# Kernel tuning notes

Hardware: AMD Instinct MI355X
Metric: run time of the kernel (lower is better)

## Reference

```python
import jax, jax.numpy as jnp
import numpy as np

B, T, E, H, V, O = 64, 512, 128, 256, 100000, 1


def setup_inputs() -> dict:
    key = jax.random.key(0)
    ks = jax.random.split(key, 10)
    sE, sH = 1.0 / np.sqrt(E), 1.0 / np.sqrt(H)
    return {
        "x": jax.random.randint(ks[0], (B, T), 0, V),
        "emb_table": jax.random.normal(ks[1], (V, E), jnp.float32) * 0.1,
        "W_ih": jax.random.normal(ks[2], (4 * H, E), jnp.float32) * sE,  # torch gate order i,f,g,o
        "W_hh": jax.random.normal(ks[3], (4 * H, H), jnp.float32) * sH,
        "b_ih": jnp.zeros((4 * H,), jnp.float32),  # biases init'd to 0 in source
        "b_hh": jnp.zeros((4 * H,), jnp.float32),
        "Wm": jax.random.normal(ks[4], (H, H), jnp.float32) * sH,
        "bm": jnp.zeros((H,), jnp.float32),
        "Wf": jax.random.normal(ks[5], (O, H), jnp.float32) * sH,
        "bf": jnp.zeros((O,), jnp.float32),
    }


def reference(x, emb_table, W_ih, W_hh, b_ih, b_hh, Wm, bm, Wf, bf):
    batch = x.shape[0]
    hid = W_hh.shape[1]
    # vectorized replacement for the per-(i,j) python-loop embedding copy
    embeds = emb_table[x]                                  # [B,T,E]
    # precompute input contribution to all gates for every timestep
    gx = jnp.einsum('bte,ge->btg', embeds, W_ih) + b_ih     # [B,T,4H]
    gx = jnp.swapaxes(gx, 0, 1)                             # [T,B,4H]
    h0 = jnp.zeros((batch, hid), embeds.dtype)
    c0 = jnp.zeros((batch, hid), embeds.dtype)

    def step(carry, g_t):
        h, c = carry
        g = g_t + h @ W_hh.T + b_hh                         # [B,4H]
        i, f, gg, o = jnp.split(g, 4, axis=-1)
        i, f, o = jax.nn.sigmoid(i), jax.nn.sigmoid(f), jax.nn.sigmoid(o)
        c = f * c + i * jnp.tanh(gg)
        h = o * jnp.tanh(c)
        return (h, c), h

    (hT, cT), hs = jax.lax.scan(step, (h0, c0), gx)
    out = jnp.swapaxes(hs, 0, 1)                            # [B,T,H]
    out = out @ Wm.T + bm                                   # ffmiddle
    out = out @ Wf.T + bf                                   # fc -> [B,T,O]
    sig_out = jax.nn.sigmoid(out).reshape(batch, -1).mean(axis=1)  # [B]
    # hidden = (h_n, c_n) with leading num_layers=1 dim, as in torch
    return sig_out, hT[None, :, :], cT[None, :, :]
```

## Files before the change

kernel.cpp:

```cpp
#include <hip/hip_runtime.h>


#define BATCH 64
#define TSTEPS 512
#define EDIM 128
#define HDIM 256
#define G4H 1024

typedef short bf16x8 __attribute__((ext_vector_type(8)));
typedef short bf16x4 __attribute__((ext_vector_type(4)));
typedef float f32x4 __attribute__((ext_vector_type(4)));

__device__ __forceinline__ unsigned short f2bf(float f) {
  unsigned u = __builtin_bit_cast(unsigned, f);
  return (unsigned short)((u + 0x7fffu + ((u >> 16) & 1u)) >> 16);
}
__device__ __forceinline__ float bf2f(unsigned short h) {
  unsigned u = ((unsigned)h) << 16;
  return __builtin_bit_cast(float, u);
}
__device__ __forceinline__ unsigned pk2(float a, float b) {
  return (unsigned)f2bf(a) | ((unsigned)f2bf(b) << 16);
}
__device__ __forceinline__ float fsig(float x) {
  return __builtin_amdgcn_rcpf(1.f + __expf(-x));
}
__device__ __forceinline__ float ftanh(float x) {
  return 1.f - 2.f * __builtin_amdgcn_rcpf(__expf(2.f * x) + 1.f);
}
__device__ __forceinline__ bf16x8 ldfrag(const unsigned short* p) {
  bf16x4 a = *(const bf16x4*)p;
  bf16x4 b = *(const bf16x4*)(p + 16);
  return __builtin_shufflevector(a, b, 0, 1, 2, 3, 4, 5, 6, 7);
}
__device__ __forceinline__ bf16x8 pack8(float4 v0, float4 v1) {
  bf16x8 f;
  f[0] = (short)f2bf(v0.x); f[1] = (short)f2bf(v0.y);
  f[2] = (short)f2bf(v0.z); f[3] = (short)f2bf(v0.w);
  f[4] = (short)f2bf(v1.x); f[5] = (short)f2bf(v1.y);
  f[6] = (short)f2bf(v1.z); f[7] = (short)f2bf(v1.w);
  return f;
}

__global__ __launch_bounds__(256) void k_gx(const int* __restrict__ x,
                                            const float* __restrict__ emb,
                                            const float* __restrict__ Wih,
                                            const float* __restrict__ bih,
                                            unsigned short* __restrict__ gx3) {
  const int t = blockIdx.x;
  const int g0 = blockIdx.y * 64;
  const int tid = threadIdx.x;
  __shared__ unsigned short Al[64 * 136];
  __shared__ unsigned short Bl[64 * 136];
  __shared__ int tok[64];
  if (tid < 64) tok[tid] = x[tid * TSTEPS + t];
  __syncthreads();
  {
    const int r = tid >> 2, c0 = (tid & 3) * 32;
    const float* asrc = emb + (size_t)tok[r] * EDIM + c0;
    const float* bsrc = Wih + (size_t)(g0 + r) * EDIM + c0;
#pragma unroll
    for (int s = 0; s < 32; s += 8) {
      float4 a0 = *(const float4*)(asrc + s);
      float4 a1 = *(const float4*)(asrc + s + 4);
      uint4 pa = {pk2(a0.x, a0.y), pk2(a0.z, a0.w), pk2(a1.x, a1.y), pk2(a1.z, a1.w)};
      *(uint4*)&Al[r * 136 + c0 + s] = pa;
      float4 b0 = *(const float4*)(bsrc + s);
      float4 b1 = *(const float4*)(bsrc + s + 4);
      uint4 pb = {pk2(b0.x, b0.y), pk2(b0.z, b0.w), pk2(b1.x, b1.y), pk2(b1.z, b1.w)};
      *(uint4*)&Bl[r * 136 + c0 + s] = pb;
    }
  }
  __syncthreads();
  const int lane = tid & 63, w = tid >> 6;
  const int lo = lane & 15, hi = lane >> 4;
  const int mb = (w & 1) * 32, nb = (w >> 1) * 32;
  f32x4 acc[2][2];
#pragma unroll
  for (int jj = 0; jj < 2; ++jj) {
    float bv = bih[g0 + nb + jj * 16 + lo];
    acc[0][jj] = (f32x4){bv, bv, bv, bv};
    acc[1][jj] = acc[0][jj];
  }
#pragma unroll
  for (int kk = 0; kk < 4; ++kk) {
    bf16x8 af0 = ldfrag(&Al[(mb + lo) * 136 + kk * 32 + hi * 4]);
    bf16x8 af1 = ldfrag(&Al[(mb + 16 + lo) * 136 + kk * 32 + hi * 4]);
    bf16x8 bf0 = ldfrag(&Bl[(nb + lo) * 136 + kk * 32 + hi * 4]);
    bf16x8 bf1 = ldfrag(&Bl[(nb + 16 + lo) * 136 + kk * 32 + hi * 4]);
    acc[0][0] = __builtin_amdgcn_mfma_f32_16x16x32_bf16(af0, bf0, acc[0][0], 0, 0, 0);
    acc[0][1] = __builtin_amdgcn_mfma_f32_16x16x32_bf16(af0, bf1, acc[0][1], 0, 0, 0);
    acc[1][0] = __builtin_amdgcn_mfma_f32_16x16x32_bf16(af1, bf0, acc[1][0], 0, 0, 0);
    acc[1][1] = __builtin_amdgcn_mfma_f32_16x16x32_bf16(af1, bf1, acc[1][1], 0, 0, 0);
  }
#pragma unroll
  for (int i = 0; i < 2; ++i)
#pragma unroll
    for (int jj = 0; jj < 2; ++jj) {
      int grp = (w & 1) * 2 + i;
      int col = g0 + nb + jj * 16 + lo;
      int g = col >> 8, jc = col & 255;
      int halfb = jc >> 7, wv = (jc >> 4) & 7, lov = jc & 15;
      size_t base = (((size_t)(t * 8 + grp * 2 + halfb) * 8 + wv) * 64 +
                     (hi * 16 + lov)) * 16 + g * 4;
      unsigned long long val =
          (unsigned long long)pk2(acc[i][jj][0], acc[i][jj][1]) |
          ((unsigned long long)pk2(acc[i][jj][2], acc[i][jj][3]) << 32);
      *(unsigned long long*)&gx3[base] = val;
    }
}

__global__ __launch_bounds__(512, 2) void k_rec(const unsigned short* __restrict__ gx3,
                                                const float* __restrict__ Whh,
                                                const float* __restrict__ bhh,
                                                const float* __restrict__ weff,
                                                unsigned long long* __restrict__ hx,
                                                float* __restrict__ out) {
  const int tid = threadIdx.x;
  const int bp = blockIdx.x;
  const int grp = bp >> 1, half = bp & 1;
  const int b0 = grp * 16;
  const int lane = tid & 63, w = tid >> 6;
  const int lo = lane & 15, hi = lane >> 4;
  const int j = half * 128 + w * 16 + lo;
  __shared__ unsigned short h_lds[2][32 * 136];
  bf16x8 wf[4][8];
  float bhv[4];
#pragma unroll
  for (int g = 0; g < 4; ++g) {
    const float* wr = Whh + (size_t)(g * 256 + j) * HDIM;
    bhv[g] = bhh[g * 256 + j];
#pragma unroll
    for (int kk = 0; kk < 8; ++kk) {
      const float* p = wr + kk * 32 + hi * 8;
      wf[g][kk] = pack8(*(const float4*)p, *(const float4*)(p + 4));
    }
  }
  const int hb_b = tid >> 5, hb_g = tid & 31;
  float wv8[8];
#pragma unroll
  for (int e = 0; e < 8; ++e) wv8[e] = weff[hb_g * 8 + e];
  const float c0 = weff[256];
  float sig_acc = 0.f;
  for (int i = tid; i < 32 * 136 / 2; i += 512) ((unsigned*)h_lds[0])[i] = 0u;
  const unsigned short* gp = gx3 + (((size_t)bp * 8 + w) * 64 + lane) * 16;
  unsigned gwA[8], gwB[8];
  {
    uint4 a = *(const uint4*)(gp);
    uint4 b = *(const uint4*)(gp + 8);
    gwA[0] = a.x; gwA[1] = a.y; gwA[2] = a.z; gwA[3] = a.w;
    gwA[4] = b.x; gwA[5] = b.y; gwA[6] = b.z; gwA[7] = b.w;
    uint4 c2 = *(const uint4*)(gp + 65536);
    uint4 d2 = *(const uint4*)(gp + 65536 + 8);
    gwB[0] = c2.x; gwB[1] = c2.y; gwB[2] = c2.z; gwB[3] = c2.w;
    gwB[4] = d2.x; gwB[5] = d2.y; gwB[6] = d2.z; gwB[7] = d2.w;
  }
  float c[4] = {0.f, 0.f, 0.f, 0.f};
  float hv[4];
  const int ob = (j >> 3) * 136 + (j & 7);
  const int jp = ((half ^ 1) * 128) + ((tid >> 6) << 4) + (tid & 15);
  const int hip = (tid >> 4) & 3;
  const int pb = (jp >> 3) * 136 + (jp & 7);
  __syncthreads();
  auto step = [&](int t, unsigned (&G)[8]) {
    const int cur = t & 1, nxt = cur ^ 1;
    const unsigned wt = (unsigned)(t + 1);
    f32x4 acc[4];
#pragma unroll
    for (int g = 0; g < 4; ++g)
#pragma unroll
      for (int r = 0; r < 4; ++r) {
        unsigned word = G[g * 2 + (r >> 1)];
        unsigned short v = (r & 1) ? (unsigned short)(word >> 16) : (unsigned short)word;
        acc[g][r] = bf2f(v) + bhv[g];
      }
#pragma unroll
    for (int kk = 0; kk < 8; ++kk) {
      bf16x8 a = *(const bf16x8*)&h_lds[cur][(kk * 4 + hi) * 136 + lo * 8];
      acc[0] = __builtin_amdgcn_mfma_f32_16x16x32_bf16(a, wf[0][kk], acc[0], 0, 0, 0);
      acc[1] = __builtin_amdgcn_mfma_f32_16x16x32_bf16(a, wf[1][kk], acc[1], 0, 0, 0);
      acc[2] = __builtin_amdgcn_mfma_f32_16x16x32_bf16(a, wf[2][kk], acc[2], 0, 0, 0);
      acc[3] = __builtin_amdgcn_mfma_f32_16x16x32_bf16(a, wf[3][kk], acc[3], 0, 0, 0);
    }
    unsigned short hbf[4];
#pragma unroll
    for (int r = 0; r < 4; ++r) {
      float iv = fsig(acc[0][r]), fv = fsig(acc[1][r]);
      float gv = ftanh(acc[2][r]), ov = fsig(acc[3][r]);
      c[r] = fv * c[r] + iv * gv;
      hv[r] = ov * ftanh(c[r]);
      hbf[r] = f2bf(hv[r]);
    }
    const int par = (int)(wt & 1u);
    {
      const unsigned long long tg = ((unsigned long long)wt) << 32;
      unsigned long long* dst = &hx[((size_t)(par * 8 + bp)) * 1024 + w * 128 + lane * 2];
      __hip_atomic_store(&dst[0], tg | (unsigned long long)pk2(hv[0], hv[1]),
                         __ATOMIC_RELAXED, __HIP_MEMORY_SCOPE_AGENT);
      __hip_atomic_store(&dst[1], tg | (unsigned long long)pk2(hv[2], hv[3]),
                         __ATOMIC_RELAXED, __HIP_MEMORY_SCOPE_AGENT);
      asm volatile("" ::: "memory");
    }
#pragma unroll
    for (int r = 0; r < 4; ++r) h_lds[nxt][ob + (hi * 4 + r) * 8] = hbf[r];
    unsigned long long v0, v1;
    {
      unsigned long long* src = &hx[((size_t)(par * 8 + (bp ^ 1))) * 1024 + tid * 2];
      do {
        v0 = __hip_atomic_load(&src[0], __ATOMIC_RELAXED, __HIP_MEMORY_SCOPE_AGENT);
        v1 = __hip_atomic_load(&src[1], __ATOMIC_RELAXED, __HIP_MEMORY_SCOPE_AGENT);
      } while ((unsigned)(v0 >> 32) != wt || (unsigned)(v1 >> 32) != wt);
    }
    if (t + 2 < TSTEPS) {
      const unsigned short* q = gp + (size_t)(t + 2) * 65536;
      uint4 a = *(const uint4*)(q);
      uint4 b = *(const uint4*)(q + 8);
      G[0] = a.x; G[1] = a.y; G[2] = a.z; G[3] = a.w;
      G[4] = b.x; G[5] = b.y; G[6] = b.z; G[7] = b.w;
    }
    h_lds[nxt][pb + (hip * 4 + 0) * 8] = (unsigned short)v0;
    h_lds[nxt][pb + (hip * 4 + 1) * 8] = (unsigned short)(v0 >> 16);
    h_lds[nxt][pb + (hip * 4 + 2) * 8] = (unsigned short)v1;
    h_lds[nxt][pb + (hip * 4 + 3) * 8] = (unsigned short)(v1 >> 16);
    __syncthreads();
    {
      bf16x8 hh = *(const bf16x8*)&h_lds[nxt][hb_g * 136 + hb_b * 8];
      float s = 0.f;
#pragma unroll
      for (int e = 0; e < 8; ++e) s += bf2f((unsigned short)hh[e]) * wv8[e];
      s += __shfl_xor(s, 1);  s += __shfl_xor(s, 2);  s += __shfl_xor(s, 4);
      s += __shfl_xor(s, 8);  s += __shfl_xor(s, 16);
      sig_acc += fsig(s + c0);
    }
  };
  for (int t = 0; t < TSTEPS; t += 2) {
    step(t, gwA);
    step(t + 1, gwB);
  }
  if (half == 0 && hb_g == 0) out[b0 + hb_b] = sig_acc * (1.f / 512.f);
#pragma unroll
  for (int r = 0; r < 4; ++r) {
    const int b = b0 + hi * 4 + r;
    out[64 + b * HDIM + j] = hv[r];
    out[64 + BATCH * HDIM + b * HDIM + j] = c[r];
  }
}

__global__ __launch_bounds__(256) void k_weff(const float* __restrict__ Wm,
                                              const float* __restrict__ bm,
                                              const float* __restrict__ Wf,
                                              const float* __restrict__ bfb,
                                              float* __restrict__ weff) {
  const int k = threadIdx.x;
  __shared__ float red[256];
  float acc = 0.f;
#pragma unroll 8
  for (int jj = 0; jj < 256; ++jj) acc += Wf[jj] * Wm[jj * 256 + k];
  weff[k] = acc;
  red[k] = bm[k] * Wf[k];
  __syncthreads();
  for (int s = 128; s > 0; s >>= 1) {
    if (k < s) red[k] += red[k + s];
    __syncthreads();
  }
  if (k == 0) weff[256] = red[0] + bfb[0];
}

extern "C" void kernel_launch(void* const* d_in, const int* in_sizes, int n_in,
                              void* d_out, int out_size, void* d_ws, size_t ws_size,
                              hipStream_t stream) {
  (void)in_sizes; (void)n_in; (void)out_size; (void)ws_size;
  const int* x = (const int*)d_in[0];
  const float* emb = (const float*)d_in[1];
  const float* Wih = (const float*)d_in[2];
  const float* Whh = (const float*)d_in[3];
  const float* bih = (const float*)d_in[4];
  const float* bhh = (const float*)d_in[5];
  const float* Wm  = (const float*)d_in[6];
  const float* bm  = (const float*)d_in[7];
  const float* Wf  = (const float*)d_in[8];
  const float* bf  = (const float*)d_in[9];
  float* out = (float*)d_out;
  char* ws = (char*)d_ws;
  const size_t gx_bytes = (size_t)TSTEPS * BATCH * G4H * 2;
  const size_t hx_bytes = (size_t)2 * 8 * 1024 * 8;
  unsigned short* gx3 = (unsigned short*)ws;
  unsigned long long* hx = (unsigned long long*)(ws + gx_bytes);
  float* weff = (float*)(ws + gx_bytes + hx_bytes);
  hipMemsetAsync(hx, 0, hx_bytes, stream);
  k_gx<<<dim3(512, 16), 256, 0, stream>>>(x, emb, Wih, bih, gx3);
  k_weff<<<1, 256, 0, stream>>>(Wm, bm, Wf, bf, weff);
  k_rec<<<8, 512, 0, stream>>>(gx3, Whh, bhh, weff, hx, out);
}
```

Baseline: 1.197 ms.

## Split recurrent MFMA into own/partner halves to overlap with cross-block exchange

Each LSTM step's h@W_hh product is split into the K-half this block computes itself and the half received from the partner block. The own-half MFMAs for the next step now run before polling for the partner's hidden state, and the head reduction is moved into that gap. This hides exchange latency behind compute. The poll loop is also software-pipelined with two outstanding load pairs. It adds a second barrier per step and a more intricate prologue and epilogue, which brings some risk of ordering mistakes.

```diff
diff --git a/kernel.cpp b/kernel.cpp
--- a/kernel.cpp
+++ b/kernel.cpp
@@ -144,28 +144,27 @@
   float sig_acc = 0.f;
   for (int i = tid; i < 32 * 136 / 2; i += 512) ((unsigned*)h_lds[0])[i] = 0u;
   const unsigned short* gp = gx3 + (((size_t)bp * 8 + w) * 64 + lane) * 16;
-  unsigned gwA[8], gwB[8];
+  unsigned gwE[8], gwO[8];
   {
     uint4 a = *(const uint4*)(gp);
     uint4 b = *(const uint4*)(gp + 8);
-    gwA[0] = a.x; gwA[1] = a.y; gwA[2] = a.z; gwA[3] = a.w;
-    gwA[4] = b.x; gwA[5] = b.y; gwA[6] = b.z; gwA[7] = b.w;
+    gwE[0] = a.x; gwE[1] = a.y; gwE[2] = a.z; gwE[3] = a.w;
+    gwE[4] = b.x; gwE[5] = b.y; gwE[6] = b.z; gwE[7] = b.w;
     uint4 c2 = *(const uint4*)(gp + 65536);
     uint4 d2 = *(const uint4*)(gp + 65536 + 8);
-    gwB[0] = c2.x; gwB[1] = c2.y; gwB[2] = c2.z; gwB[3] = c2.w;
-    gwB[4] = d2.x; gwB[5] = d2.y; gwB[6] = d2.z; gwB[7] = d2.w;
+    gwO[0] = c2.x; gwO[1] = c2.y; gwO[2] = c2.z; gwO[3] = c2.w;
+    gwO[4] = d2.x; gwO[5] = d2.y; gwO[6] = d2.z; gwO[7] = d2.w;
   }
   float c[4] = {0.f, 0.f, 0.f, 0.f};
   float hv[4];
+  f32x4 acc[4];
   const int ob = (j >> 3) * 136 + (j & 7);
   const int jp = ((half ^ 1) * 128) + ((tid >> 6) << 4) + (tid & 15);
   const int hip = (tid >> 4) & 3;
   const int pb = (jp >> 3) * 136 + (jp & 7);
   __syncthreads();
-  auto step = [&](int t, unsigned (&G)[8]) {
-    const int cur = t & 1, nxt = cur ^ 1;
-    const unsigned wt = (unsigned)(t + 1);
-    f32x4 acc[4];
+
+  auto cinit = [&](const unsigned (&G)[8]) {
 #pragma unroll
     for (int g = 0; g < 4; ++g)
 #pragma unroll
@@ -174,14 +173,47 @@
         unsigned short v = (r & 1) ? (unsigned short)(word >> 16) : (unsigned short)word;
         acc[g][r] = bf2f(v) + bhv[g];
       }
-#pragma unroll
-    for (int kk = 0; kk < 8; ++kk) {
-      bf16x8 a = *(const bf16x8*)&h_lds[cur][(kk * 4 + hi) * 136 + lo * 8];
-      acc[0] = __builtin_amdgcn_mfma_f32_16x16x32_bf16(a, wf[0][kk], acc[0], 0, 0, 0);
-      acc[1] = __builtin_amdgcn_mfma_f32_16x16x32_bf16(a, wf[1][kk], acc[1], 0, 0, 0);
-      acc[2] = __builtin_amdgcn_mfma_f32_16x16x32_bf16(a, wf[2][kk], acc[2], 0, 0, 0);
-      acc[3] = __builtin_amdgcn_mfma_f32_16x16x32_bf16(a, wf[3][kk], acc[3], 0, 0, 0);
-    }
+  };
+  auto mfma_own = [&](int buf) {
+    if (half == 0) {
+#pragma unroll
+      for (int kk = 0; kk < 4; ++kk) {
+        bf16x8 a = *(const bf16x8*)&h_lds[buf][(kk * 4 + hi) * 136 + lo * 8];
+#pragma unroll
+        for (int g = 0; g < 4; ++g)
+          acc[g] = __builtin_amdgcn_mfma_f32_16x16x32_bf16(a, wf[g][kk], acc[g], 0, 0, 0);
+      }
+    } else {
+#pragma unroll
+      for (int kk = 4; kk < 8; ++kk) {
+        bf16x8 a = *(const bf16x8*)&h_lds[buf][(kk * 4 + hi) * 136 + lo * 8];
+#pragma unroll
+        for (int g = 0; g < 4; ++g)
+          acc[g] = __builtin_amdgcn_mfma_f32_16x16x32_bf16(a, wf[g][kk], acc[g], 0, 0, 0);
+      }
+    }
+  };
+  auto mfma_par = [&](int buf) {
+    if (half == 0) {
+#pragma unroll
+      for (int kk = 4; kk < 8; ++kk) {
+        bf16x8 a = *(const bf16x8*)&h_lds[buf][(kk * 4 + hi) * 136 + lo * 8];
+#pragma unroll
+        for (int g = 0; g < 4; ++g)
+          acc[g] = __builtin_amdgcn_mfma_f32_16x16x32_bf16(a, wf[g][kk], acc[g], 0, 0, 0);
+      }
+    } else {
+#pragma unroll
+      for (int kk = 0; kk < 4; ++kk) {
+        bf16x8 a = *(const bf16x8*)&h_lds[buf][(kk * 4 + hi) * 136 + lo * 8];
+#pragma unroll
+        for (int g = 0; g < 4; ++g)
+          acc[g] = __builtin_amdgcn_mfma_f32_16x16x32_bf16(a, wf[g][kk], acc[g], 0, 0, 0);
+      }
+    }
+  };
+  auto update_store = [&](int t) {
+    const unsigned wt = (unsigned)(t + 1);
     unsigned short hbf[4];
 #pragma unroll
     for (int r = 0; r < 4; ++r) {
@@ -192,51 +224,80 @@
       hbf[r] = f2bf(hv[r]);
     }
     const int par = (int)(wt & 1u);
-    {
-      const unsigned long long tg = ((unsigned long long)wt) << 32;
-      unsigned long long* dst = &hx[((size_t)(par * 8 + bp)) * 1024 + w * 128 + lane * 2];
-      __hip_atomic_store(&dst[0], tg | (unsigned long long)pk2(hv[0], hv[1]),
-                         __ATOMIC_RELAXED, __HIP_MEMORY_SCOPE_AGENT);
-      __hip_atomic_store(&dst[1], tg | (unsigned long long)pk2(hv[2], hv[3]),
-                         __ATOMIC_RELAXED, __HIP_MEMORY_SCOPE_AGENT);
-      asm volatile("" ::: "memory");
-    }
-#pragma unroll
-    for (int r = 0; r < 4; ++r) h_lds[nxt][ob + (hi * 4 + r) * 8] = hbf[r];
+    unsigned long long* dst = &hx[((size_t)(par * 8 + bp)) * 1024 + w * 128 + lane * 2];
+    const unsigned long long tg = ((unsigned long long)wt) << 32;
+    __hip_atomic_store(&dst[0], tg | (unsigned long long)pk2(hv[0], hv[1]),
+                       __ATOMIC_RELAXED, __HIP_MEMORY_SCOPE_AGENT);
+    __hip_atomic_store(&dst[1], tg | (unsigned long long)pk2(hv[2], hv[3]),
+                       __ATOMIC_RELAXED, __HIP_MEMORY_SCOPE_AGENT);
+    asm volatile("" ::: "memory");
+#pragma unroll
+    for (int r = 0; r < 4; ++r) h_lds[par][ob + (hi * 4 + r) * 8] = hbf[r];
+  };
+  auto head = [&](int buf) {
+    bf16x8 hh = *(const bf16x8*)&h_lds[buf][hb_g * 136 + hb_b * 8];
+    float s = 0.f;
+#pragma unroll
+    for (int e = 0; e < 8; ++e) s += bf2f((unsigned short)hh[e]) * wv8[e];
+    s += __shfl_xor(s, 1);  s += __shfl_xor(s, 2);  s += __shfl_xor(s, 4);
+    s += __shfl_xor(s, 8);  s += __shfl_xor(s, 16);
+    sig_acc += fsig(s + c0);
+  };
+  auto gx_issue = [&](int s, unsigned (&G)[8]) {
+    const unsigned short* q = gp + (size_t)s * 65536;
+    uint4 a = *(const uint4*)(q);
+    uint4 b = *(const uint4*)(q + 8);
+    G[0] = a.x; G[1] = a.y; G[2] = a.z; G[3] = a.w;
+    G[4] = b.x; G[5] = b.y; G[6] = b.z; G[7] = b.w;
+  };
+  auto poll_write = [&](int t) {
+    const unsigned wt = (unsigned)(t + 1);
+    const int par = (int)(wt & 1u);
+    unsigned long long* src = &hx[((size_t)(par * 8 + (bp ^ 1))) * 1024 + tid * 2];
+    unsigned long long a0 = __hip_atomic_load(&src[0], __ATOMIC_RELAXED, __HIP_MEMORY_SCOPE_AGENT);
+    unsigned long long a1 = __hip_atomic_load(&src[1], __ATOMIC_RELAXED, __HIP_MEMORY_SCOPE_AGENT);
+    unsigned long long b0 = __hip_atomic_load(&src[0], __ATOMIC_RELAXED, __HIP_MEMORY_SCOPE_AGENT);
+    unsigned long long b1 = __hip_atomic_load(&src[1], __ATOMIC_RELAXED, __HIP_MEMORY_SCOPE_AGENT);
     unsigned long long v0, v1;
-    {
-      unsigned long long* src = &hx[((size_t)(par * 8 + (bp ^ 1))) * 1024 + tid * 2];
-      do {
-        v0 = __hip_atomic_load(&src[0], __ATOMIC_RELAXED, __HIP_MEMORY_SCOPE_AGENT);
-        v1 = __hip_atomic_load(&src[1], __ATOMIC_RELAXED, __HIP_MEMORY_SCOPE_AGENT);
-      } while ((unsigned)(v0 >> 32) != wt || (unsigned)(v1 >> 32) != wt);
-    }
-    if (t + 2 < TSTEPS) {
-      const unsigned short* q = gp + (size_t)(t + 2) * 65536;
-      uint4 a = *(const uint4*)(q);
-      uint4 b = *(const uint4*)(q + 8);
-      G[0] = a.x; G[1] = a.y; G[2] = a.z; G[3] = a.w;
-      G[4] = b.x; G[5] = b.y; G[6] = b.z; G[7] = b.w;
-    }
-    h_lds[nxt][pb + (hip * 4 + 0) * 8] = (unsigned short)v0;
-    h_lds[nxt][pb + (hip * 4 + 1) * 8] = (unsigned short)(v0 >> 16);
-    h_lds[nxt][pb + (hip * 4 + 2) * 8] = (unsigned short)v1;
-    h_lds[nxt][pb + (hip * 4 + 3) * 8] = (unsigned short)(v1 >> 16);
+    for (;;) {
+      if ((unsigned)(a0 >> 32) == wt && (unsigned)(a1 >> 32) == wt) { v0 = a0; v1 = a1; break; }
+      a0 = b0; a1 = b1;
+      b0 = __hip_atomic_load(&src[0], __ATOMIC_RELAXED, __HIP_MEMORY_SCOPE_AGENT);
+      b1 = __hip_atomic_load(&src[1], __ATOMIC_RELAXED, __HIP_MEMORY_SCOPE_AGENT);
+    }
+    h_lds[par][pb + (hip * 4 + 0) * 8] = (unsigned short)v0;
+    h_lds[par][pb + (hip * 4 + 1) * 8] = (unsigned short)(v0 >> 16);
+    h_lds[par][pb + (hip * 4 + 2) * 8] = (unsigned short)v1;
+    h_lds[par][pb + (hip * 4 + 3) * 8] = (unsigned short)(v1 >> 16);
+  };
+  auto body = [&](int t, unsigned (&Gc)[8], unsigned (&Gf)[8]) {
+    mfma_par(t & 1);
+    update_store(t);
+    if (t + 2 < TSTEPS) gx_issue(t + 2, Gf);
     __syncthreads();
-    {
-      bf16x8 hh = *(const bf16x8*)&h_lds[nxt][hb_g * 136 + hb_b * 8];
-      float s = 0.f;
-#pragma unroll
-      for (int e = 0; e < 8; ++e) s += bf2f((unsigned short)hh[e]) * wv8[e];
-      s += __shfl_xor(s, 1);  s += __shfl_xor(s, 2);  s += __shfl_xor(s, 4);
-      s += __shfl_xor(s, 8);  s += __shfl_xor(s, 16);
-      sig_acc += fsig(s + c0);
-    }
-  };
-  for (int t = 0; t < TSTEPS; t += 2) {
-    step(t, gwA);
-    step(t + 1, gwB);
-  }
+    if (t < TSTEPS - 1) {
+      cinit(Gc);
+      mfma_own((t + 1) & 1);
+    }
+    head(t & 1);
+    poll_write(t);
+    __syncthreads();
+  };
+
+  cinit(gwE);
+  update_store(0);
+  gx_issue(2, gwE);
+  __syncthreads();
+  cinit(gwO);
+  mfma_own(1);
+  poll_write(0);
+  __syncthreads();
+  for (int t = 1; t + 1 < TSTEPS - 1; t += 2) {
+    body(t, gwE, gwO);
+    body(t + 1, gwO, gwE);
+  }
+  body(TSTEPS - 1, gwE, gwO);
+  head(0);
   if (half == 0 && hb_g == 0) out[b0 + hb_b] = sig_acc * (1.f / 512.f);
 #pragma unroll
   for (int r = 0; r < 4; ++r) {
```

Result: faster. 1.034 ms, median of 2 (-13.6%).

## Quantize recurrent matmul to int8 MFMA and drop cross-block hidden exchange

Applied to the files above, without the earlier changes.

The recurrence kernel now quantizes W_hh per row to int8 and the hidden state per step to int8 with a dynamic block-wide max scale, using i8 MFMA instead of bf16. Each block owns all 256 hidden units for 16 batch rows, so the two-block split with atomic spin-wait exchange through global memory is removed and only 4 blocks launch. The b_hh bias is folded into the precomputed input gates. This removes the inter-block synchronisation latency per step but adds an extra __syncthreads for the max reduction and introduces int8 quantization error in the recurrence.

```diff
diff --git a/kernel.cpp b/kernel.cpp
--- a/kernel.cpp
+++ b/kernel.cpp
@@ -10,6 +10,7 @@
 typedef short bf16x8 __attribute__((ext_vector_type(8)));
 typedef short bf16x4 __attribute__((ext_vector_type(4)));
 typedef float f32x4 __attribute__((ext_vector_type(4)));
+typedef int i32x4 __attribute__((ext_vector_type(4)));
 
 __device__ __forceinline__ unsigned short f2bf(float f) {
   unsigned u = __builtin_bit_cast(unsigned, f);
@@ -33,20 +34,18 @@
   bf16x4 b = *(const bf16x4*)(p + 16);
   return __builtin_shufflevector(a, b, 0, 1, 2, 3, 4, 5, 6, 7);
 }
-__device__ __forceinline__ bf16x8 pack8(float4 v0, float4 v1) {
-  bf16x8 f;
-  f[0] = (short)f2bf(v0.x); f[1] = (short)f2bf(v0.y);
-  f[2] = (short)f2bf(v0.z); f[3] = (short)f2bf(v0.w);
-  f[4] = (short)f2bf(v1.x); f[5] = (short)f2bf(v1.y);
-  f[6] = (short)f2bf(v1.z); f[7] = (short)f2bf(v1.w);
-  return f;
+__device__ __forceinline__ int q8(float v, float qs) {
+  float r = __builtin_rintf(v * qs);
+  r = fmaxf(-127.f, fminf(127.f, r));
+  return (int)r;
 }
 
 __global__ __launch_bounds__(256) void k_gx(const int* __restrict__ x,
                                             const float* __restrict__ emb,
                                             const float* __restrict__ Wih,
                                             const float* __restrict__ bih,
-                                            unsigned short* __restrict__ gx3) {
+                                            const float* __restrict__ bhh,
+                                            unsigned short* __restrict__ gx4) {
   const int t = blockIdx.x;
   const int g0 = blockIdx.y * 64;
   const int tid = threadIdx.x;
@@ -78,7 +77,8 @@
   f32x4 acc[2][2];
 #pragma unroll
   for (int jj = 0; jj < 2; ++jj) {
-    float bv = bih[g0 + nb + jj * 16 + lo];
+    const int col = g0 + nb + jj * 16 + lo;
+    float bv = bih[col] + bhh[col];
     acc[0][jj] = (f32x4){bv, bv, bv, bv};
     acc[1][jj] = acc[0][jj];
   }
@@ -97,153 +97,182 @@
   for (int i = 0; i < 2; ++i)
 #pragma unroll
     for (int jj = 0; jj < 2; ++jj) {
-      int grp = (w & 1) * 2 + i;
-      int col = g0 + nb + jj * 16 + lo;
-      int g = col >> 8, jc = col & 255;
-      int halfb = jc >> 7, wv = (jc >> 4) & 7, lov = jc & 15;
-      size_t base = (((size_t)(t * 8 + grp * 2 + halfb) * 8 + wv) * 64 +
-                     (hi * 16 + lov)) * 16 + g * 4;
+      const int o = (w & 1) * 2 + i;
+      const int col = g0 + nb + jj * 16 + lo;
+      const int g = col >> 8, rem = col & 255;
+      const int w4 = rem >> 5, t2 = (rem >> 4) & 1;
+      size_t idx = ((((size_t)t * 4 + o) * 8 + w4) * 64 + (hi * 16 + lo)) * 32 +
+                   (g * 2 + t2) * 4;
       unsigned long long val =
           (unsigned long long)pk2(acc[i][jj][0], acc[i][jj][1]) |
           ((unsigned long long)pk2(acc[i][jj][2], acc[i][jj][3]) << 32);
-      *(unsigned long long*)&gx3[base] = val;
-    }
-}
-
-__global__ __launch_bounds__(512, 2) void k_rec(const unsigned short* __restrict__ gx3,
-                                                const float* __restrict__ Whh,
-                                                const float* __restrict__ bhh,
-                                                const float* __restrict__ weff,
-                                                unsigned long long* __restrict__ hx,
-                                                float* __restrict__ out) {
+      *(unsigned long long*)&gx4[idx] = val;
+    }
+}
+
+__global__ __launch_bounds__(512) void k_rec(const unsigned short* __restrict__ gx4,
+                                             const float* __restrict__ Whh,
+                                             const float* __restrict__ weff,
+                                             float* __restrict__ out) {
   const int tid = threadIdx.x;
-  const int bp = blockIdx.x;
-  const int grp = bp >> 1, half = bp & 1;
-  const int b0 = grp * 16;
+  const int blk = blockIdx.x;
   const int lane = tid & 63, w = tid >> 6;
   const int lo = lane & 15, hi = lane >> 4;
-  const int j = half * 128 + w * 16 + lo;
-  __shared__ unsigned short h_lds[2][32 * 136];
-  bf16x8 wf[4][8];
-  float bhv[4];
-#pragma unroll
-  for (int g = 0; g < 4; ++g) {
-    const float* wr = Whh + (size_t)(g * 256 + j) * HDIM;
-    bhv[g] = bhh[g * 256 + j];
-#pragma unroll
-    for (int kk = 0; kk < 8; ++kk) {
-      const float* p = wr + kk * 32 + hi * 8;
-      wf[g][kk] = pack8(*(const float4*)p, *(const float4*)(p + 4));
-    }
-  }
-  const int hb_b = tid >> 5, hb_g = tid & 31;
+  __shared__ unsigned char h8[2][16 * 272];
+  __shared__ float mxl[8];
+  i32x4 wq[4][2][4];
+  float sW[4][2];
+#pragma unroll
+  for (int g = 0; g < 4; ++g)
+#pragma unroll
+    for (int t2 = 0; t2 < 2; ++t2) {
+      const float* wr = Whh + (size_t)(g * 256 + w * 32 + t2 * 16 + lo) * HDIM;
+      float m = 0.f;
+#pragma unroll 16
+      for (int e = 0; e < 64; ++e) {
+        float4 v = *(const float4*)(wr + e * 4);
+        m = fmaxf(m, fmaxf(fmaxf(fabsf(v.x), fabsf(v.y)),
+                           fmaxf(fabsf(v.z), fabsf(v.w))));
+      }
+      m = fmaxf(m, 1e-20f);
+      sW[g][t2] = m * (1.f / 127.f);
+      const float qs = 127.f / m;
+#pragma unroll
+      for (int kk = 0; kk < 4; ++kk) {
+        int wd[4];
+#pragma unroll
+        for (int u2 = 0; u2 < 4; ++u2) {
+          float4 v = *(const float4*)(wr + kk * 64 + hi * 16 + u2 * 4);
+          int b0 = q8(v.x, qs), b1 = q8(v.y, qs), b2 = q8(v.z, qs), b3 = q8(v.w, qs);
+          wd[u2] = (b0 & 255) | ((b1 & 255) << 8) | ((b2 & 255) << 16) | ((b3 & 255) << 24);
+        }
+        wq[g][t2][kk] = (i32x4){wd[0], wd[1], wd[2], wd[3]};
+      }
+    }
+  const int hb_b = tid >> 5, hsub = tid & 31;
+  const int hgr = hsub >> 1, heh = (hsub & 1) * 8;
   float wv8[8];
 #pragma unroll
-  for (int e = 0; e < 8; ++e) wv8[e] = weff[hb_g * 8 + e];
+  for (int e = 0; e < 8; ++e) wv8[e] = weff[hgr * 16 + heh + e];
   const float c0 = weff[256];
   float sig_acc = 0.f;
-  for (int i = tid; i < 32 * 136 / 2; i += 512) ((unsigned*)h_lds[0])[i] = 0u;
-  const unsigned short* gp = gx3 + (((size_t)bp * 8 + w) * 64 + lane) * 16;
-  unsigned gwA[8], gwB[8];
+  for (int i = tid; i < 16 * 272 / 4; i += 512) ((unsigned*)h8[0])[i] = 0u;
+  float c[2][4] = {{0.f, 0.f, 0.f, 0.f}, {0.f, 0.f, 0.f, 0.f}};
+  float hv[2][4];
+  float sHp = 0.f;
+  const unsigned short* gp = gx4 + ((((size_t)blk) * 8 + w) * 64 + (hi * 16 + lo)) * 32;
+  unsigned GA[16], GB[16];
   {
     uint4 a = *(const uint4*)(gp);
     uint4 b = *(const uint4*)(gp + 8);
-    gwA[0] = a.x; gwA[1] = a.y; gwA[2] = a.z; gwA[3] = a.w;
-    gwA[4] = b.x; gwA[5] = b.y; gwA[6] = b.z; gwA[7] = b.w;
-    uint4 c2 = *(const uint4*)(gp + 65536);
-    uint4 d2 = *(const uint4*)(gp + 65536 + 8);
-    gwB[0] = c2.x; gwB[1] = c2.y; gwB[2] = c2.z; gwB[3] = c2.w;
-    gwB[4] = d2.x; gwB[5] = d2.y; gwB[6] = d2.z; gwB[7] = d2.w;
-  }
-  float c[4] = {0.f, 0.f, 0.f, 0.f};
-  float hv[4];
-  const int ob = (j >> 3) * 136 + (j & 7);
-  const int jp = ((half ^ 1) * 128) + ((tid >> 6) << 4) + (tid & 15);
-  const int hip = (tid >> 4) & 3;
-  const int pb = (jp >> 3) * 136 + (jp & 7);
+    uint4 c2 = *(const uint4*)(gp + 16);
+    uint4 d2 = *(const uint4*)(gp + 24);
+    GA[0] = a.x;  GA[1] = a.y;  GA[2] = a.z;  GA[3] = a.w;
+    GA[4] = b.x;  GA[5] = b.y;  GA[6] = b.z;  GA[7] = b.w;
+    GA[8] = c2.x; GA[9] = c2.y; GA[10] = c2.z; GA[11] = c2.w;
+    GA[12] = d2.x; GA[13] = d2.y; GA[14] = d2.z; GA[15] = d2.w;
+  }
   __syncthreads();
-  auto step = [&](int t, unsigned (&G)[8]) {
+
+  auto step = [&](int t, unsigned (&Gc)[16], unsigned (&Gn)[16]) {
     const int cur = t & 1, nxt = cur ^ 1;
-    const unsigned wt = (unsigned)(t + 1);
-    f32x4 acc[4];
+    i32x4 acc[4][2];
 #pragma unroll
     for (int g = 0; g < 4; ++g)
 #pragma unroll
-      for (int r = 0; r < 4; ++r) {
-        unsigned word = G[g * 2 + (r >> 1)];
-        unsigned short v = (r & 1) ? (unsigned short)(word >> 16) : (unsigned short)word;
-        acc[g][r] = bf2f(v) + bhv[g];
-      }
-#pragma unroll
-    for (int kk = 0; kk < 8; ++kk) {
-      bf16x8 a = *(const bf16x8*)&h_lds[cur][(kk * 4 + hi) * 136 + lo * 8];
-      acc[0] = __builtin_amdgcn_mfma_f32_16x16x32_bf16(a, wf[0][kk], acc[0], 0, 0, 0);
-      acc[1] = __builtin_amdgcn_mfma_f32_16x16x32_bf16(a, wf[1][kk], acc[1], 0, 0, 0);
-      acc[2] = __builtin_amdgcn_mfma_f32_16x16x32_bf16(a, wf[2][kk], acc[2], 0, 0, 0);
-      acc[3] = __builtin_amdgcn_mfma_f32_16x16x32_bf16(a, wf[3][kk], acc[3], 0, 0, 0);
-    }
-    unsigned short hbf[4];
-#pragma unroll
-    for (int r = 0; r < 4; ++r) {
-      float iv = fsig(acc[0][r]), fv = fsig(acc[1][r]);
-      float gv = ftanh(acc[2][r]), ov = fsig(acc[3][r]);
-      c[r] = fv * c[r] + iv * gv;
-      hv[r] = ov * ftanh(c[r]);
-      hbf[r] = f2bf(hv[r]);
-    }
-    const int par = (int)(wt & 1u);
-    {
-      const unsigned long long tg = ((unsigned long long)wt) << 32;
-      unsigned long long* dst = &hx[((size_t)(par * 8 + bp)) * 1024 + w * 128 + lane * 2];
-      __hip_atomic_store(&dst[0], tg | (unsigned long long)pk2(hv[0], hv[1]),
-                         __ATOMIC_RELAXED, __HIP_MEMORY_SCOPE_AGENT);
-      __hip_atomic_store(&dst[1], tg | (unsigned long long)pk2(hv[2], hv[3]),
-                         __ATOMIC_RELAXED, __HIP_MEMORY_SCOPE_AGENT);
-      asm volatile("" ::: "memory");
-    }
-#pragma unroll
-    for (int r = 0; r < 4; ++r) h_lds[nxt][ob + (hi * 4 + r) * 8] = hbf[r];
-    unsigned long long v0, v1;
-    {
-      unsigned long long* src = &hx[((size_t)(par * 8 + (bp ^ 1))) * 1024 + tid * 2];
-      do {
-        v0 = __hip_atomic_load(&src[0], __ATOMIC_RELAXED, __HIP_MEMORY_SCOPE_AGENT);
-        v1 = __hip_atomic_load(&src[1], __ATOMIC_RELAXED, __HIP_MEMORY_SCOPE_AGENT);
-      } while ((unsigned)(v0 >> 32) != wt || (unsigned)(v1 >> 32) != wt);
-    }
-    if (t + 2 < TSTEPS) {
-      const unsigned short* q = gp + (size_t)(t + 2) * 65536;
+      for (int t2 = 0; t2 < 2; ++t2) acc[g][t2] = (i32x4){0, 0, 0, 0};
+#pragma unroll
+    for (int kk = 0; kk < 4; ++kk) {
+      i32x4 af = *(const i32x4*)&h8[cur][(kk * 4 + hi) * 272 + lo * 16];
+#pragma unroll
+      for (int g = 0; g < 4; ++g) {
+        acc[g][0] = __builtin_amdgcn_mfma_i32_16x16x64_i8(af, wq[g][0][kk], acc[g][0], 0, 0, 0);
+        acc[g][1] = __builtin_amdgcn_mfma_i32_16x16x64_i8(af, wq[g][1][kk], acc[g][1], 0, 0, 0);
+      }
+    }
+    if (t + 1 < TSTEPS) {
+      const unsigned short* q = gp + (size_t)(t + 1) * 65536;
       uint4 a = *(const uint4*)(q);
       uint4 b = *(const uint4*)(q + 8);
-      G[0] = a.x; G[1] = a.y; G[2] = a.z; G[3] = a.w;
-      G[4] = b.x; G[5] = b.y; G[6] = b.z; G[7] = b.w;
-    }
-    h_lds[nxt][pb + (hip * 4 + 0) * 8] = (unsigned short)v0;
-    h_lds[nxt][pb + (hip * 4 + 1) * 8] = (unsigned short)(v0 >> 16);
-    h_lds[nxt][pb + (hip * 4 + 2) * 8] = (unsigned short)v1;
-    h_lds[nxt][pb + (hip * 4 + 3) * 8] = (unsigned short)(v1 >> 16);
+      uint4 c2 = *(const uint4*)(q + 16);
+      uint4 d2 = *(const uint4*)(q + 24);
+      Gn[0] = a.x;  Gn[1] = a.y;  Gn[2] = a.z;  Gn[3] = a.w;
+      Gn[4] = b.x;  Gn[5] = b.y;  Gn[6] = b.z;  Gn[7] = b.w;
+      Gn[8] = c2.x; Gn[9] = c2.y; Gn[10] = c2.z; Gn[11] = c2.w;
+      Gn[12] = d2.x; Gn[13] = d2.y; Gn[14] = d2.z; Gn[15] = d2.w;
+    }
+    float scg[4][2];
+#pragma unroll
+    for (int g = 0; g < 4; ++g)
+#pragma unroll
+      for (int t2 = 0; t2 < 2; ++t2) scg[g][t2] = sW[g][t2] * sHp;
+    float mx = 0.f;
+#pragma unroll
+    for (int t2 = 0; t2 < 2; ++t2)
+#pragma unroll
+      for (int r = 0; r < 4; ++r) {
+        float gates[4];
+#pragma unroll
+        for (int g = 0; g < 4; ++g) {
+          const int q = g * 2 + t2;
+          unsigned word = Gc[q * 2 + (r >> 1)];
+          unsigned short gv16 = (r & 1) ? (unsigned short)(word >> 16)
+                                        : (unsigned short)word;
+          gates[g] = bf2f(gv16) + (float)acc[g][t2][r] * scg[g][t2];
+        }
+        float iv = fsig(gates[0]), fv = fsig(gates[1]);
+        float gg = ftanh(gates[2]), ov = fsig(gates[3]);
+        c[t2][r] = fv * c[t2][r] + iv * gg;
+        hv[t2][r] = ov * ftanh(c[t2][r]);
+        mx = fmaxf(mx, fabsf(hv[t2][r]));
+      }
+    mx = fmaxf(mx, __shfl_xor(mx, 1));  mx = fmaxf(mx, __shfl_xor(mx, 2));
+    mx = fmaxf(mx, __shfl_xor(mx, 4));  mx = fmaxf(mx, __shfl_xor(mx, 8));
+    mx = fmaxf(mx, __shfl_xor(mx, 16)); mx = fmaxf(mx, __shfl_xor(mx, 32));
+    if (lane == 0) mxl[w] = mx;
+    __syncthreads();
+    float bm = fmaxf(fmaxf(fmaxf(mxl[0], mxl[1]), fmaxf(mxl[2], mxl[3])),
+                     fmaxf(fmaxf(mxl[4], mxl[5]), fmaxf(mxl[6], mxl[7])));
+    bm = fmaxf(bm, 1e-8f);
+    const float sHn = bm * (1.f / 127.f);
+    const float rq = 127.f / bm;
+#pragma unroll
+    for (int t2 = 0; t2 < 2; ++t2)
+#pragma unroll
+      for (int r = 0; r < 4; ++r) {
+        int qv = q8(hv[t2][r], rq);
+        h8[nxt][(w * 2 + t2) * 272 + (hi * 4 + r) * 16 + lo] = (unsigned char)(qv & 255);
+      }
     __syncthreads();
     {
-      bf16x8 hh = *(const bf16x8*)&h_lds[nxt][hb_g * 136 + hb_b * 8];
+      unsigned long long hb8 =
+          *(const unsigned long long*)&h8[nxt][hgr * 272 + hb_b * 16 + heh];
       float s = 0.f;
 #pragma unroll
-      for (int e = 0; e < 8; ++e) s += bf2f((unsigned short)hh[e]) * wv8[e];
+      for (int e = 0; e < 8; ++e)
+        s += (float)((signed char)(hb8 >> (8 * e))) * wv8[e];
+      s *= sHn;
       s += __shfl_xor(s, 1);  s += __shfl_xor(s, 2);  s += __shfl_xor(s, 4);
       s += __shfl_xor(s, 8);  s += __shfl_xor(s, 16);
       sig_acc += fsig(s + c0);
     }
+    sHp = sHn;
   };
+
   for (int t = 0; t < TSTEPS; t += 2) {
-    step(t, gwA);
-    step(t + 1, gwB);
-  }
-  if (half == 0 && hb_g == 0) out[b0 + hb_b] = sig_acc * (1.f / 512.f);
-#pragma unroll
-  for (int r = 0; r < 4; ++r) {
-    const int b = b0 + hi * 4 + r;
-    out[64 + b * HDIM + j] = hv[r];
-    out[64 + BATCH * HDIM + b * HDIM + j] = c[r];
-  }
+    step(t, GA, GB);
+    step(t + 1, GB, GA);
+  }
+  if ((tid & 31) == 0) out[blk * 16 + hb_b] = sig_acc * (1.f / 512.f);
+#pragma unroll
+  for (int t2 = 0; t2 < 2; ++t2)
+#pragma unroll
+    for (int r = 0; r < 4; ++r) {
+      const int b = blk * 16 + hi * 4 + r;
+      const int u = w * 32 + t2 * 16 + lo;
+      out[64 + b * HDIM + u] = hv[t2][r];
+      out[64 + BATCH * HDIM + b * HDIM + u] = c[t2][r];
+    }
 }
 
 __global__ __launch_bounds__(256) void k_weff(const float* __restrict__ Wm,
@@ -283,12 +312,9 @@
   float* out = (float*)d_out;
   char* ws = (char*)d_ws;
   const size_t gx_bytes = (size_t)TSTEPS * BATCH * G4H * 2;
-  const size_t hx_bytes = (size_t)2 * 8 * 1024 * 8;
-  unsigned short* gx3 = (unsigned short*)ws;
-  unsigned long long* hx = (unsigned long long*)(ws + gx_bytes);
-  float* weff = (float*)(ws + gx_bytes + hx_bytes);
-  hipMemsetAsync(hx, 0, hx_bytes, stream);
-  k_gx<<<dim3(512, 16), 256, 0, stream>>>(x, emb, Wih, bih, gx3);
+  unsigned short* gx4 = (unsigned short*)ws;
+  float* weff = (float*)(ws + gx_bytes);
+  k_gx<<<dim3(512, 16), 256, 0, stream>>>(x, emb, Wih, bih, bhh, gx4);
   k_weff<<<1, 256, 0, stream>>>(Wm, bm, Wf, bf, weff);
-  k_rec<<<8, 512, 0, stream>>>(gx3, Whh, bhh, weff, hx, out);
-}
+  k_rec<<<4, 512, 0, stream>>>(gx4, Whh, weff, out);
+}
```

Measured after the change: 1.684 ms. +40.6%, slower.
